# Performance work log

Hardware: AMD Instinct MI355X
Metric: run time of the kernel (lower is better)

The kernel has to match this reference:

```python
import jax, jax.numpy as jnp
import numpy as np
import math

B, L, H, D = 4, 2048, 8, 64
FACTOR = 5
SAMPLE_K = min(FACTOR * int(np.ceil(np.log(L))), L)  # U_part = 40
N_TOP = min(FACTOR * int(np.ceil(np.log(L))), L)     # u = 40


def setup_inputs() -> dict:
    key = jax.random.key(0)
    kq, kk, kv, ki = jax.random.split(key, 4)
    queries = jax.random.normal(kq, (B, L, H, D), dtype=jnp.float32)
    keys = jax.random.normal(kk, (B, L, H, D), dtype=jnp.float32)
    values = jax.random.normal(kv, (B, L, H, D), dtype=jnp.float32)
    # ProbSparse random key sampling indices (torch.randint(L_K, (L_Q, sample_k)))
    index_sample = jax.random.randint(ki, (L, SAMPLE_K), 0, L, dtype=jnp.int64)
    return {"queries": queries, "keys": keys, "values": values,
            "index_sample": index_sample}


def reference(queries, keys, values, index_sample):
    # [B, L, H, D] -> [B, H, L, D]
    Q = jnp.transpose(queries, (0, 2, 1, 3))
    K = jnp.transpose(keys, (0, 2, 1, 3))
    V = jnp.transpose(values, (0, 2, 1, 3))
    L_K = K.shape[2]

    # --- _prob_QK ---
    # gather sampled keys per query: [B, H, L_Q, sample_k, D]
    K_sample = K[:, :, index_sample, :]
    # sampled QK dots: [B, H, L_Q, sample_k]
    Q_K_sample = jnp.einsum('bhld,bhlsd->bhls', Q, K_sample)
    # sparsity measurement M = max - mean
    M = Q_K_sample.max(axis=-1) - Q_K_sample.sum(axis=-1) / L_K  # [B, H, L_Q]
    _, M_top = jax.lax.top_k(M, N_TOP)  # [B, H, n_top]
    # gather top queries: [B, H, n_top, D]
    Q_reduce = jnp.take_along_axis(Q, M_top[..., None], axis=2)
    # reduced scores against all keys: [B, H, n_top, L_K]
    scores_top = jnp.einsum('bhud,bhkd->bhuk', Q_reduce, K)

    # --- forward tail ---
    scale = 1.0 / math.sqrt(D)
    attn = jax.nn.softmax(scores_top * scale, axis=-1)  # dropout = identity (eval)
    context = jnp.einsum('bhuk,bhkd->bhud', attn, V)  # [B, H, n_top, D]
    # [B, n_top, H, D]
    return jnp.transpose(context, (0, 2, 1, 3))
```

## Files before the change

### kernel.cpp

```cpp
#include <hip/hip_runtime.h>
#include <hip/hip_bf16.h>

#define BB 4
#define LL 2048
#define HH 8
#define DD 64
#define SK 40
#define NT 40
#define CH 256
#define NCH (LL / CH)
#define QH 20

#define WS 10
#define HB 68
#define RS (HH * HB)

__global__ __launch_bounds__(256) void compute_m_kernel(
        const float* __restrict__ Q, const float* __restrict__ K,
        const int* __restrict__ idx, float* __restrict__ M) {
    __shared__ float kbuf[4][2][2 * RS];
    __shared__ int sidx[SK];
    __shared__ float2 mlpart[4][HH];

    int blk = blockIdx.x;
    int x = blk & 7, g = blk >> 3;
    int b = x >> 1;
    int l = (g << 1) | (x & 1);
    int t = threadIdx.x;

    if (t < SK) sidx[t] = idx[(size_t)l * SK + t];

    int lane = t & 63, w = t >> 6;
    int s_lo = lane >> 5;
    int h    = (lane >> 2) & 7;
    int q    = lane & 3;

    const float4* Qb = (const float4*)(Q + ((size_t)b * LL + l) * 512 + h * 64 + q * 16);
    float4 qf0 = Qb[0], qf1 = Qb[1], qf2 = Qb[2], qf3 = Qb[3];

    const float* Kb = K + (size_t)b * LL * 512;

    int r  = lane >> 5;
    int cw = lane & 31;
    int av = cw >> 4;
    int c4 = (4 * cw) & 63;
    __syncthreads();

    float4 ra0, ra1, ra2, ra3;
    float4 rb0, rb1, rb2, rb3;

    #define LOADX(p, d0, d1, d2, d3) do {                                       \
        const float* src = Kb + (size_t)sidx[w * WS + (p) * 2 + r] * 512        \
                         + cw * 4;                                              \
        d0 = *(const float4*)(src);                                             \
        d1 = *(const float4*)(src + 128);                                       \
        d2 = *(const float4*)(src + 256);                                       \
        d3 = *(const float4*)(src + 384);                                       \
    } while (0)
    #define WRITEX(slot, d0, d1, d2, d3) do {                                   \
        float* base = &kbuf[w][slot][r * RS + c4];                              \
        *(float4*)(base + (av + 0) * HB) = d0;                                  \
        *(float4*)(base + (av + 2) * HB) = d1;                                  \
        *(float4*)(base + (av + 4) * HB) = d2;                                  \
        *(float4*)(base + (av + 6) * HB) = d3;                                  \
    } while (0)
    #define CONSUME(slot) do {                                                  \
        asm volatile("s_waitcnt lgkmcnt(0)" ::: "memory");                      \
        const float* kb = &kbuf[w][slot][s_lo * RS + h * HB + q * 16];          \
        float4 k0 = *(const float4*)(kb);                                       \
        float4 k1 = *(const float4*)(kb + 4);                                   \
        float4 k2 = *(const float4*)(kb + 8);                                   \
        float4 k3 = *(const float4*)(kb + 12);                                  \
        float pd = qf0.x*k0.x + qf0.y*k0.y + qf0.z*k0.z + qf0.w*k0.w            \
                 + qf1.x*k1.x + qf1.y*k1.y + qf1.z*k1.z + qf1.w*k1.w            \
                 + qf2.x*k2.x + qf2.y*k2.y + qf2.z*k2.z + qf2.w*k2.w            \
                 + qf3.x*k3.x + qf3.y*k3.y + qf3.z*k3.z + qf3.w*k3.w;           \
        pd += __shfl_xor(pd, 1, 64);                                            \
        pd += __shfl_xor(pd, 2, 64);                                            \
        mx = fmaxf(mx, pd);                                                     \
        sm += pd;                                                               \
    } while (0)

    float mx = -INFINITY, sm = 0.0f;

    LOADX(0, ra0, ra1, ra2, ra3);
    LOADX(1, rb0, rb1, rb2, rb3);
    WRITEX(0, ra0, ra1, ra2, ra3);

    LOADX(2, ra0, ra1, ra2, ra3);
    CONSUME(0);
    WRITEX(1, rb0, rb1, rb2, rb3);

    LOADX(3, rb0, rb1, rb2, rb3);
    CONSUME(1);
    WRITEX(0, ra0, ra1, ra2, ra3);

    LOADX(4, ra0, ra1, ra2, ra3);
    CONSUME(0);
    WRITEX(1, rb0, rb1, rb2, rb3);

    CONSUME(1);
    WRITEX(0, ra0, ra1, ra2, ra3);

    CONSUME(0);

    #undef LOADX
    #undef WRITEX
    #undef CONSUME

    mx = fmaxf(mx, __shfl_xor(mx, 32, 64));
    sm += __shfl_xor(sm, 32, 64);

    if ((lane & 0x23) == 0)
        mlpart[w][h] = make_float2(mx, sm);
    __syncthreads();

    if (t < HH) {
        float MX = -INFINITY, SM = 0.0f;
        #pragma unroll
        for (int w2 = 0; w2 < 4; ++w2) {
            float2 ml = mlpart[w2][t];
            MX = fmaxf(MX, ml.x);
            SM += ml.y;
        }
        M[((size_t)b * HH + t) * LL + l] = MX - SM * (1.0f / (float)LL);
    }
}

__global__ __launch_bounds__(256) void topk_kernel(const float* __restrict__ M,
                                                   int* __restrict__ topi) {
    __shared__ unsigned long long keys[LL];
    __shared__ unsigned long long wmax[4];
    __shared__ int win;
    int bh = blockIdx.x;
    int t  = threadIdx.x;
    int lane = t & 63, w = t >> 6;

    unsigned long long kmax = 0ULL;
    #pragma unroll
    for (int j = 0; j < 8; ++j) {
        int i = t + 256 * j;
        unsigned int bits = __float_as_uint(M[(size_t)bh * LL + i]);
        bits = (bits & 0x80000000u) ? ~bits : (bits | 0x80000000u);
        unsigned long long k = ((unsigned long long)bits << 11)
                             | (unsigned int)(LL - 1 - i);
        keys[i] = k;
        if (k > kmax) kmax = k;
    }
    __syncthreads();

    for (int u = 0; u < NT; ++u) {
        unsigned long long k = kmax;
        #pragma unroll
        for (int off = 32; off >= 1; off >>= 1) {
            unsigned long long o = __shfl_xor(k, off, 64);
            if (o > k) k = o;
        }
        if (lane == 0) wmax[w] = k;
        __syncthreads();
        if (t == 0) {
            unsigned long long k0 = wmax[0];
            if (wmax[1] > k0) k0 = wmax[1];
            if (wmax[2] > k0) k0 = wmax[2];
            if (wmax[3] > k0) k0 = wmax[3];
            int i = (LL - 1) - (int)(k0 & 0x7FF);
            topi[bh * NT + u] = i;
            keys[i] = 0ULL;
            win = i;
        }
        __syncthreads();
        if ((win & 255) == t) {
            kmax = 0ULL;
            #pragma unroll
            for (int j = 0; j < 8; ++j) {
                unsigned long long kk = keys[t + 256 * j];
                if (kk > kmax) kmax = kk;
            }
        }
    }
}

__global__ __launch_bounds__(256, 3) void attn_kernel(
        const float* __restrict__ Q, const float* __restrict__ K,
        const float* __restrict__ V, const int* __restrict__ topi,
        float2* __restrict__ pml, float* __restrict__ po) {
    __shared__ float  qs[QH][DD];
    __shared__ float4 e4buf[4][64];
    __shared__ float  oarea[4][QH][DD];
    __shared__ float  mlarea[4][QH][2];

    int blk = blockIdx.x;
    int qh  = blk >> 8;
    int cc2 = blk & 255;
    int c   = cc2 & (NCH - 1);
    int bh  = cc2 >> 3;
    int h = bh & (HH - 1), b = bh >> 3;
    int t = threadIdx.x, lane = t & 63, w = t >> 6;
    int u0 = qh * QH;

    for (int i = t; i < QH * DD; i += 256) {
        int u = i >> 6, d = i & 63;
        int lq = topi[bh * NT + u0 + u];
        qs[u][d] = Q[(((size_t)b * LL + lq) * HH + h) * DD + d];
    }

    int key = c * CH + w * 64 + lane;
    const float4* kr = (const float4*)&K[(((size_t)b * LL + key) * HH + h) * DD];
    float4 kreg[16];
    #pragma unroll
    for (int j = 0; j < 16; ++j) kreg[j] = kr[j];

    float vcol[64];
    const float* vb = &V[(((size_t)b * LL + c * CH + w * 64) * HH + h) * DD + lane];
    #pragma unroll
    for (int j = 0; j < 64; ++j) vcol[j] = vb[(size_t)j * HH * DD];

    __syncthreads();

    for (int uq = 0; uq < QH / 4; ++uq) {
        float o0 = 0, o1 = 0, o2 = 0, o3 = 0;
        float mv0, mv1, mv2, mv3, lv0, lv1, lv2, lv3;
        float4 ev;
        #pragma unroll
        for (int j = 0; j < 4; ++j) {
            int u = uq * 4 + j;
            const float4* q4 = (const float4*)&qs[u][0];
            float s = 0.0f;
            #pragma unroll
            for (int cc = 0; cc < 16; ++cc) {
                float4 qv = q4[cc];
                s += qv.x * kreg[cc].x + qv.y * kreg[cc].y
                   + qv.z * kreg[cc].z + qv.w * kreg[cc].w;
            }
            s *= 0.125f;
            float m = s;
            #pragma unroll
            for (int off = 32; off >= 1; off >>= 1)
                m = fmaxf(m, __shfl_xor(m, off, 64));
            float e = __expf(s - m);
            float ls = e;
            #pragma unroll
            for (int off = 32; off >= 1; off >>= 1)
                ls += __shfl_xor(ls, off, 64);
            if (j == 0) { mv0 = m; lv0 = ls; ev.x = e; }
            if (j == 1) { mv1 = m; lv1 = ls; ev.y = e; }
            if (j == 2) { mv2 = m; lv2 = ls; ev.z = e; }
            if (j == 3) { mv3 = m; lv3 = ls; ev.w = e; }
        }
        e4buf[w][lane] = ev;
        asm volatile("s_waitcnt lgkmcnt(0)" ::: "memory");
        #pragma unroll
        for (int l2 = 0; l2 < 64; ++l2) {
            float4 e = e4buf[w][l2];
            float  v = vcol[l2];
            o0 += e.x * v; o1 += e.y * v; o2 += e.z * v; o3 += e.w * v;
        }
        oarea[w][uq * 4 + 0][lane] = o0;
        oarea[w][uq * 4 + 1][lane] = o1;
        oarea[w][uq * 4 + 2][lane] = o2;
        oarea[w][uq * 4 + 3][lane] = o3;
        if (lane == 0) {
            mlarea[w][uq * 4 + 0][0] = mv0; mlarea[w][uq * 4 + 0][1] = lv0;
            mlarea[w][uq * 4 + 1][0] = mv1; mlarea[w][uq * 4 + 1][1] = lv1;
            mlarea[w][uq * 4 + 2][0] = mv2; mlarea[w][uq * 4 + 2][1] = lv2;
            mlarea[w][uq * 4 + 3][0] = mv3; mlarea[w][uq * 4 + 3][1] = lv3;
        }
    }
    __syncthreads();

    for (int i = t; i < QH * DD; i += 256) {
        int u = i >> 6, d = i & 63;
        float m0 = mlarea[0][u][0], m1 = mlarea[1][u][0];
        float m2 = mlarea[2][u][0], m3 = mlarea[3][u][0];
        float mb = fmaxf(fmaxf(m0, m1), fmaxf(m2, m3));
        float s0 = __expf(m0 - mb), s1 = __expf(m1 - mb);
        float s2 = __expf(m2 - mb), s3 = __expf(m3 - mb);
        float ob = oarea[0][u][d] * s0 + oarea[1][u][d] * s1
                 + oarea[2][u][d] * s2 + oarea[3][u][d] * s3;
        int gu = u0 + u;
        po[((size_t)(bh * NT + gu) * NCH + c) * DD + d] = ob;
        if (d == 0) {
            float lb = mlarea[0][u][1] * s0 + mlarea[1][u][1] * s1
                     + mlarea[2][u][1] * s2 + mlarea[3][u][1] * s3;
            pml[(bh * NT + gu) * NCH + c] = make_float2(mb, lb);
        }
    }
}

__global__ __launch_bounds__(256) void merge_kernel(
        const float2* __restrict__ pml, const float* __restrict__ po,
        float* __restrict__ out) {
    int wid  = blockIdx.x * 4 + (threadIdx.x >> 6);
    int lane = threadIdx.x & 63;
    int u  = wid % NT;
    int bh = wid / NT;
    int h = bh & (HH - 1), b = bh >> 3;
    int base = (bh * NT + u) * NCH;

    float m = -INFINITY;
    #pragma unroll
    for (int cc = 0; cc < NCH; ++cc) m = fmaxf(m, pml[base + cc].x);
    float lsum = 0.0f, o = 0.0f;
    #pragma unroll
    for (int cc = 0; cc < NCH; ++cc) {
        float2 ml = pml[base + cc];
        float sc = __expf(ml.x - m);
        lsum += ml.y * sc;
        o    += po[(size_t)(base + cc) * DD + lane] * sc;
    }
    out[(((size_t)b * NT + u) * HH + h) * DD + lane] = o / lsum;
}

extern "C" void kernel_launch(void* const* d_in, const int* in_sizes, int n_in,
                              void* d_out, int out_size, void* d_ws, size_t ws_size,
                              hipStream_t stream) {
    const float* Q   = (const float*)d_in[0];
    const float* K   = (const float*)d_in[1];
    const float* V   = (const float*)d_in[2];
    const int*   idx = (const int*)d_in[3];
    float* out = (float*)d_out;

    char* ws = (char*)d_ws;
    float*  M    = (float*)ws;                        ws += (size_t)BB * HH * LL * sizeof(float);
    int*    topi = (int*)ws;                          ws += (size_t)BB * HH * NT * sizeof(int);
    float2* pml  = (float2*)ws;                       ws += (size_t)BB * HH * NT * NCH * sizeof(float2);
    float*  po   = (float*)ws;

    hipLaunchKernelGGL(compute_m_kernel, dim3(BB * LL), dim3(256), 0, stream,
                       Q, K, idx, M);
    hipLaunchKernelGGL(topk_kernel, dim3(BB * HH), dim3(256), 0, stream, M, topi);
    hipLaunchKernelGGL(attn_kernel, dim3(2 * BB * HH * NCH), dim3(256), 0, stream,
                       Q, K, V, topi, pml, po);
    hipLaunchKernelGGL(merge_kernel, dim3(BB * HH * NT / 4), dim3(256), 0, stream,
                       pml, po, out);
}
```

Before: 167.5 us.

## Load sampled keys directly into registers, dropping LDS staging in compute_m

The M-computation kernel no longer stages gathered K rows through a double-buffered shared-memory transpose. Each lane now reads its own 16-float slice of each of its 5 sampled key rows straight from global memory into registers and computes the dot products there. All 5 rows are issued up front to keep more loads in flight, and launch bounds now request 4 blocks per SM. This removes the LDS writes and reads and the waitcnt stalls, but raises register pressure and changes the global access pattern to 64-byte per-lane chunks.

```diff
diff --git a/kernel.cpp b/kernel.cpp
--- a/kernel.cpp
+++ b/kernel.cpp
@@ -12,14 +12,10 @@
 #define QH 20
 
 #define WS 10
-#define HB 68
-#define RS (HH * HB)
-
-__global__ __launch_bounds__(256) void compute_m_kernel(
+
+__global__ __launch_bounds__(256, 4) void compute_m_kernel(
         const float* __restrict__ Q, const float* __restrict__ K,
         const int* __restrict__ idx, float* __restrict__ M) {
-    __shared__ float kbuf[4][2][2 * RS];
-    __shared__ int sidx[SK];
     __shared__ float2 mlpart[4][HH];
 
     int blk = blockIdx.x;
@@ -27,9 +23,6 @@
     int b = x >> 1;
     int l = (g << 1) | (x & 1);
     int t = threadIdx.x;
-
-    if (t < SK) sidx[t] = idx[(size_t)l * SK + t];
-
     int lane = t & 63, w = t >> 6;
     int s_lo = lane >> 5;
     int h    = (lane >> 2) & 7;
@@ -38,75 +31,39 @@
     const float4* Qb = (const float4*)(Q + ((size_t)b * LL + l) * 512 + h * 64 + q * 16);
     float4 qf0 = Qb[0], qf1 = Qb[1], qf2 = Qb[2], qf3 = Qb[3];
 
-    const float* Kb = K + (size_t)b * LL * 512;
-
-    int r  = lane >> 5;
-    int cw = lane & 31;
-    int av = cw >> 4;
-    int c4 = (4 * cw) & 63;
-    __syncthreads();
-
-    float4 ra0, ra1, ra2, ra3;
-    float4 rb0, rb1, rb2, rb3;
-
-    #define LOADX(p, d0, d1, d2, d3) do {                                       \
-        const float* src = Kb + (size_t)sidx[w * WS + (p) * 2 + r] * 512        \
-                         + cw * 4;                                              \
-        d0 = *(const float4*)(src);                                             \
-        d1 = *(const float4*)(src + 128);                                       \
-        d2 = *(const float4*)(src + 256);                                       \
-        d3 = *(const float4*)(src + 384);                                       \
-    } while (0)
-    #define WRITEX(slot, d0, d1, d2, d3) do {                                   \
-        float* base = &kbuf[w][slot][r * RS + c4];                              \
-        *(float4*)(base + (av + 0) * HB) = d0;                                  \
-        *(float4*)(base + (av + 2) * HB) = d1;                                  \
-        *(float4*)(base + (av + 4) * HB) = d2;                                  \
-        *(float4*)(base + (av + 6) * HB) = d3;                                  \
-    } while (0)
-    #define CONSUME(slot) do {                                                  \
-        asm volatile("s_waitcnt lgkmcnt(0)" ::: "memory");                      \
-        const float* kb = &kbuf[w][slot][s_lo * RS + h * HB + q * 16];          \
-        float4 k0 = *(const float4*)(kb);                                       \
-        float4 k1 = *(const float4*)(kb + 4);                                   \
-        float4 k2 = *(const float4*)(kb + 8);                                   \
-        float4 k3 = *(const float4*)(kb + 12);                                  \
-        float pd = qf0.x*k0.x + qf0.y*k0.y + qf0.z*k0.z + qf0.w*k0.w            \
-                 + qf1.x*k1.x + qf1.y*k1.y + qf1.z*k1.z + qf1.w*k1.w            \
-                 + qf2.x*k2.x + qf2.y*k2.y + qf2.z*k2.z + qf2.w*k2.w            \
-                 + qf3.x*k3.x + qf3.y*k3.y + qf3.z*k3.z + qf3.w*k3.w;           \
-        pd += __shfl_xor(pd, 1, 64);                                            \
-        pd += __shfl_xor(pd, 2, 64);                                            \
-        mx = fmaxf(mx, pd);                                                     \
-        sm += pd;                                                               \
-    } while (0)
+    const float* Kb = K + (size_t)b * LL * 512 + (lane & 31) * 16;
+    const int* ib = idx + (size_t)l * SK + w * WS + s_lo;
+
+    int ks[5];
+    #pragma unroll
+    for (int p = 0; p < 5; ++p) ks[p] = ib[2 * p];
+
+    float4 kd[5][4];
+    #pragma unroll
+    for (int p = 0; p < 5; ++p) {
+        const float4* src = (const float4*)(Kb + (size_t)ks[p] * 512);
+        kd[p][0] = src[0];
+        kd[p][1] = src[1];
+        kd[p][2] = src[2];
+        kd[p][3] = src[3];
+    }
 
     float mx = -INFINITY, sm = 0.0f;
-
-    LOADX(0, ra0, ra1, ra2, ra3);
-    LOADX(1, rb0, rb1, rb2, rb3);
-    WRITEX(0, ra0, ra1, ra2, ra3);
-
-    LOADX(2, ra0, ra1, ra2, ra3);
-    CONSUME(0);
-    WRITEX(1, rb0, rb1, rb2, rb3);
-
-    LOADX(3, rb0, rb1, rb2, rb3);
-    CONSUME(1);
-    WRITEX(0, ra0, ra1, ra2, ra3);
-
-    LOADX(4, ra0, ra1, ra2, ra3);
-    CONSUME(0);
-    WRITEX(1, rb0, rb1, rb2, rb3);
-
-    CONSUME(1);
-    WRITEX(0, ra0, ra1, ra2, ra3);
-
-    CONSUME(0);
-
-    #undef LOADX
-    #undef WRITEX
-    #undef CONSUME
+    #pragma unroll
+    for (int p = 0; p < 5; ++p) {
+        float pd = qf0.x*kd[p][0].x + qf0.y*kd[p][0].y
+                 + qf0.z*kd[p][0].z + qf0.w*kd[p][0].w
+                 + qf1.x*kd[p][1].x + qf1.y*kd[p][1].y
+                 + qf1.z*kd[p][1].z + qf1.w*kd[p][1].w
+                 + qf2.x*kd[p][2].x + qf2.y*kd[p][2].y
+                 + qf2.z*kd[p][2].z + qf2.w*kd[p][2].w
+                 + qf3.x*kd[p][3].x + qf3.y*kd[p][3].y
+                 + qf3.z*kd[p][3].z + qf3.w*kd[p][3].w;
+        pd += __shfl_xor(pd, 1, 64);
+        pd += __shfl_xor(pd, 2, 64);
+        mx = fmaxf(mx, pd);
+        sm += pd;
+    }
 
     mx = fmaxf(mx, __shfl_xor(mx, 32, 64));
     sm += __shfl_xor(sm, 32, 64);
```

Result: slower. 217.2 us (+29.7%).
